# Kernel tuning notes

Measured on AMD Instinct MI355X. Metric: run time of the kernel, lower is better.

Reference implementation:

```python
import jax, jax.numpy as jnp
import numpy as np

L = 3
EPSILON = 0.01
T = 1.0
L1_EPS = 1e-12  # torch F.normalize default eps


def _cdist(x, y):
    # Euclidean pairwise distance, (b, n, d) x (b, m, d) -> (b, n, m)
    x2 = jnp.sum(x * x, axis=-1, keepdims=True)            # (b, n, 1)
    y2 = jnp.sum(y * y, axis=-1)[:, None, :]               # (b, 1, m)
    xy = jnp.einsum('bnd,bmd->bnm', x, y)                  # (b, n, m)
    return jnp.sqrt(jnp.maximum(x2 + y2 - 2.0 * xy, 0.0))


def setup_inputs() -> dict:
    key = jax.random.key(0)
    k1, k2 = jax.random.split(key)
    B, S, D = 4, 2048, 512
    A = jax.random.uniform(k1, (B, S, S), dtype=jnp.float32)
    V = jax.random.normal(k2, (B, S, D), dtype=jnp.float32)
    return {"A": A, "V": V}


def reference(A, V):
    M = jnp.matmul(A, V)  # (b, s, d)
    for _ in range(L):
        Md = jax.lax.stop_gradient(M)
        Vd = jax.lax.stop_gradient(V)
        dist = _cdist(Md, Vd)                               # (b, s, s)
        w = 1.0 / (dist + EPSILON)                          # norm == 'L2'
        ww = w * A                                          # (b, s, s)
        l1 = jnp.maximum(jnp.sum(jnp.abs(ww), axis=-1, keepdims=True), L1_EPS)
        ww_norm = ww / l1
        M = (1.0 - T) * M + T * jnp.matmul(ww_norm, V)
    return M
```

## Files before the change

### kernel.cpp

```cpp
#include <hip/hip_runtime.h>


typedef __bf16 bf16;
typedef bf16 bf16x4 __attribute__((ext_vector_type(4)));
typedef bf16 bf16x8 __attribute__((ext_vector_type(8)));
typedef float f32x4 __attribute__((ext_vector_type(4)));

#define S_DIM 2048
#define D_DIM 512
#define NB    4
#define EPSILON 0.01f

__global__ void cast_kernel(const float* __restrict__ in, bf16* __restrict__ out, int n4) {
  int i = blockIdx.x * blockDim.x + threadIdx.x;
  if (i >= n4) return;
  float4 v = ((const float4*)in)[i];
  bf16x4 o = { (bf16)v.x, (bf16)v.y, (bf16)v.z, (bf16)v.w };
  ((bf16x4*)out)[i] = o;
}

__global__ void transpose_cast_kernel(const float* __restrict__ V, bf16* __restrict__ Vt) {
  __shared__ float tile[64][68];
  int b  = blockIdx.z;
  int c0 = blockIdx.x * 64;
  int r0 = blockIdx.y * 64;
  const float* Vb = V  + (size_t)b * S_DIM * D_DIM;
  bf16*       Vtb = Vt + (size_t)b * S_DIM * D_DIM;
  int tx = threadIdx.x & 15, ty = threadIdx.x >> 4;
#pragma unroll
  for (int i = 0; i < 4; ++i) {
    int r = ty + i * 16;
    float4 v = *(const float4*)(Vb + (size_t)(r0 + r) * D_DIM + (c0 + tx * 4));
    tile[r][tx * 4 + 0] = v.x; tile[r][tx * 4 + 1] = v.y;
    tile[r][tx * 4 + 2] = v.z; tile[r][tx * 4 + 3] = v.w;
  }
  __syncthreads();
#pragma unroll
  for (int i = 0; i < 4; ++i) {
    int c = ty + i * 16;
    bf16x4 o = { (bf16)tile[tx * 4 + 0][c], (bf16)tile[tx * 4 + 1][c],
                 (bf16)tile[tx * 4 + 2][c], (bf16)tile[tx * 4 + 3][c] };
    *(bf16x4*)(Vtb + (size_t)(c0 + c) * S_DIM + (r0 + tx * 4)) = o;
  }
}

__global__ void rownorm_kernel(const bf16* __restrict__ X, float* __restrict__ out) {
  int row  = blockIdx.x * 4 + (threadIdx.x >> 6);
  int lane = threadIdx.x & 63;
  bf16x8 v = *(const bf16x8*)(X + (size_t)row * D_DIM + lane * 8);
  float s = 0.f;
#pragma unroll
  for (int i = 0; i < 8; ++i) { float f = (float)v[i]; s += f * f; }
#pragma unroll
  for (int off = 32; off > 0; off >>= 1) s += __shfl_down(s, off);
  if (lane == 0) out[row] = s;
}

template <int MODE>
__global__ __launch_bounds__(256, 4)
void gemm_kernel(const bf16* __restrict__ Amat, const bf16* __restrict__ Bmat,
                 int M, int N, int K,
                 bf16* __restrict__ Cp,
                 const float* __restrict__ m2, const float* __restrict__ v2,
                 const bf16* __restrict__ Aw, bf16* __restrict__ Wout,
                 float* __restrict__ l1) {
  int bz, ks, kbeg, kend;
  if (MODE == 4) { bz = blockIdx.z >> 1; ks = blockIdx.z & 1; kbeg = ks * (K >> 1); kend = kbeg + (K >> 1); }
  else           { bz = blockIdx.z;      ks = 0;              kbeg = 0;             kend = K; }
  const int row0 = blockIdx.y * 128;
  const int col0 = blockIdx.x * 128;
  const bf16* Ab = Amat + (size_t)bz * M * K;
  const bf16* Bb = Bmat + (size_t)bz * N * K;

  __shared__ char smem[32768];
  bf16*  ldsA = (bf16*)smem;
  bf16*  ldsB = (bf16*)(smem + 16384);
  float* ldsW = (float*)smem;

  const int tid  = threadIdx.x;
  const int wave = tid >> 6;
  const int lane = tid & 63;
  const int wr   = wave >> 1;
  const int wc   = wave & 1;
  const int q    = lane >> 4;
  const int c16  = lane & 15;

  const int srow = lane >> 3;
  const int scol = ((lane & 7) ^ srow) * 8;

  f32x4 acc[4][4] = {};

  for (int k0 = kbeg; k0 < kend; k0 += 64) {
#pragma unroll
    for (int i = 0; i < 4; ++i) {
      int slot = wave * 4 + i;
      int r = slot * 8 + srow;
      __builtin_amdgcn_global_load_lds(
          (const __attribute__((address_space(1))) void*)(Ab + (size_t)(row0 + r) * K + (k0 + scol)),
          (__attribute__((address_space(3))) void*)(ldsA + slot * 512), 16, 0, 0);
      __builtin_amdgcn_global_load_lds(
          (const __attribute__((address_space(1))) void*)(Bb + (size_t)(col0 + r) * K + (k0 + scol)),
          (__attribute__((address_space(3))) void*)(ldsB + slot * 512), 16, 0, 0);
    }
    __syncthreads();

#pragma unroll
    for (int kk = 0; kk < 2; ++kk) {
      bf16x8 afr[4], bfr[4];
#pragma unroll
      for (int mt = 0; mt < 4; ++mt) {
        int R = wr * 64 + mt * 16 + c16;
        int p = ((kk << 2) + q) ^ (c16 & 7);
        afr[mt] = *(const bf16x8*)(ldsA + (size_t)R * 64 + p * 8);
      }
#pragma unroll
      for (int nt = 0; nt < 4; ++nt) {
        int R = wc * 64 + nt * 16 + c16;
        int p = ((kk << 2) + q) ^ (c16 & 7);
        bfr[nt] = *(const bf16x8*)(ldsB + (size_t)R * 64 + p * 8);
      }
#pragma unroll
      for (int mt = 0; mt < 4; ++mt)
#pragma unroll
        for (int nt = 0; nt < 4; ++nt)
          acc[mt][nt] = __builtin_amdgcn_mfma_f32_16x16x32_bf16(afr[mt], bfr[nt], acc[mt][nt], 0, 0, 0);
    }
    __syncthreads();
  }

  const int rowBase = row0 + wr * 64 + q * 4;
  const int colBase = col0 + wc * 64 + c16;

  if (MODE == 1) {
    const float* m2b = m2 + (size_t)bz * M;
    const float* v2b = v2 + (size_t)bz * N;
    float v2v[4];
#pragma unroll
    for (int nt = 0; nt < 4; ++nt) v2v[nt] = v2b[colBase + nt * 16];
#pragma unroll
    for (int mt = 0; mt < 4; ++mt)
#pragma unroll
      for (int r = 0; r < 4; ++r) {
        float m2v = m2b[rowBase + mt * 16 + r];
#pragma unroll
        for (int nt = 0; nt < 4; ++nt) {
          float d2 = fmaxf(m2v + v2v[nt] - 2.f * acc[mt][nt][r], 0.f);
          acc[mt][nt][r] = __builtin_amdgcn_rcpf(__builtin_amdgcn_sqrtf(d2) + EPSILON);
        }
      }
  }

  const int lr  = tid >> 3;
  const int sub = tid & 7;
#pragma unroll
  for (int k = 0; k < 4; ++k) {
    __syncthreads();
    if (wr == (k >> 1)) {
#pragma unroll
      for (int m = 0; m < 2; ++m) {
        int mt = 2 * (k & 1) + m;
#pragma unroll
        for (int nt = 0; nt < 4; ++nt)
#pragma unroll
          for (int r = 0; r < 4; ++r)
            ldsW[(m * 16 + q * 4 + r) * 132 + wc * 64 + nt * 16 + c16] = acc[mt][nt][r];
      }
    }
    __syncthreads();
    int gi = row0 + 32 * k + lr;
    const float* wp = ldsW + lr * 132 + sub * 16;
    float4 w0 = *(const float4*)(wp + 0);
    float4 w1 = *(const float4*)(wp + 4);
    float4 w2 = *(const float4*)(wp + 8);
    float4 w3 = *(const float4*)(wp + 12);
    float wv_[16] = { w0.x, w0.y, w0.z, w0.w, w1.x, w1.y, w1.z, w1.w,
                      w2.x, w2.y, w2.z, w2.w, w3.x, w3.y, w3.z, w3.w };
    if (MODE == 1) {
      const bf16* Awb = Aw + (size_t)bz * M * N;
      bf16*       Wob = Wout + (size_t)bz * M * N;
      float*      l1b = l1 + (size_t)bz * M;
      const bf16* ap = Awb + (size_t)gi * N + (col0 + sub * 16);
      bf16x8 a0 = *(const bf16x8*)(ap);
      bf16x8 a1 = *(const bf16x8*)(ap + 8);
      bf16x8 o0, o1;
      float rs = 0.f;
#pragma unroll
      for (int e = 0; e < 8; ++e) {
        float x0 = wv_[e] * (float)a0[e];
        float x1 = wv_[e + 8] * (float)a1[e];
        o0[e] = (bf16)x0; o1[e] = (bf16)x1;
        rs += fabsf(x0) + fabsf(x1);
      }
      bf16* op = Wob + (size_t)gi * N + (col0 + sub * 16);
      *(bf16x8*)(op)     = o0;
      *(bf16x8*)(op + 8) = o1;
      rs += __shfl_xor(rs, 1);
      rs += __shfl_xor(rs, 2);
      rs += __shfl_xor(rs, 4);
      if (sub == 0) atomicAdd(&l1b[gi], rs);
    } else {
      bf16* Cb = Cp + ((size_t)ks * NB + bz) * ((size_t)M * N);
      bf16x8 o0, o1;
#pragma unroll
      for (int e = 0; e < 8; ++e) { o0[e] = (bf16)wv_[e]; o1[e] = (bf16)wv_[e + 8]; }
      bf16* op = Cb + (size_t)gi * N + (col0 + sub * 16);
      *(bf16x8*)(op)     = o0;
      *(bf16x8*)(op + 8) = o1;
    }
  }
}

template <int RMODE>
__global__ void reduce_kernel(const bf16* __restrict__ part, const float* __restrict__ l1,
                              bf16* __restrict__ Mo, float* __restrict__ Fo,
                              float* __restrict__ m2) {
  int wave = threadIdx.x >> 6, lane = threadIdx.x & 63;
  int rg = blockIdx.x * 4 + wave;
  const bf16* p0 = part + (size_t)rg * D_DIM + lane * 8;
  const bf16* p1 = p0 + (size_t)NB * S_DIM * D_DIM;
  bf16x8 a = *(const bf16x8*)p0;
  bf16x8 b = *(const bf16x8*)p1;
  float v[8];
#pragma unroll
  for (int e = 0; e < 8; ++e) v[e] = (float)a[e] + (float)b[e];
  float sc = 1.f;
  if (RMODE >= 1) sc = __builtin_amdgcn_rcpf(fmaxf(l1[rg], 1e-12f));
  float s = 0.f;
#pragma unroll
  for (int e = 0; e < 8; ++e) { v[e] *= sc; s += v[e] * v[e]; }
  if (RMODE == 2) {
    float4 o0 = { v[0], v[1], v[2], v[3] }, o1 = { v[4], v[5], v[6], v[7] };
    float* op = Fo + (size_t)rg * D_DIM + lane * 8;
    *(float4*)(op) = o0; *(float4*)(op + 4) = o1;
  } else {
    bf16x8 o;
#pragma unroll
    for (int e = 0; e < 8; ++e) o[e] = (bf16)v[e];
    *(bf16x8*)(Mo + (size_t)rg * D_DIM + lane * 8) = o;
#pragma unroll
    for (int off = 32; off > 0; off >>= 1) s += __shfl_xor(s, off);
    if (lane == 0) m2[rg] = s;
  }
}

extern "C" void kernel_launch(void* const* d_in, const int* in_sizes, int n_in,
                              void* d_out, int out_size, void* d_ws, size_t ws_size,
                              hipStream_t stream) {
  const float* A = (const float*)d_in[0];
  const float* V = (const float*)d_in[1];
  float* out = (float*)d_out;

  char* ws = (char*)d_ws;
  bf16* Abf = (bf16*)ws;   ws += (size_t)NB * S_DIM * S_DIM * 2;
  bf16* Vbf = (bf16*)ws;   ws += (size_t)NB * S_DIM * D_DIM * 2;
  bf16* Vt  = (bf16*)ws;   ws += (size_t)NB * S_DIM * D_DIM * 2;
  bf16* Mbf = (bf16*)ws;   ws += (size_t)NB * S_DIM * D_DIM * 2;
  bf16* Wbf = (bf16*)ws;   ws += (size_t)NB * S_DIM * S_DIM * 2;
  bf16* part = (bf16*)ws;  ws += (size_t)2 * NB * S_DIM * D_DIM * 2;
  float* v2 = (float*)ws;  ws += (size_t)NB * S_DIM * 4;
  float* m2 = (float*)ws;  ws += (size_t)NB * S_DIM * 4;
  float* l1 = (float*)ws;  ws += (size_t)NB * S_DIM * 4;

  int nA4 = NB * S_DIM * S_DIM / 4;
  int nV4 = NB * S_DIM * D_DIM / 4;
  cast_kernel<<<nA4 / 256, 256, 0, stream>>>(A, Abf, nA4);
  cast_kernel<<<nV4 / 256, 256, 0, stream>>>(V, Vbf, nV4);
  transpose_cast_kernel<<<dim3(D_DIM / 64, S_DIM / 64, NB), 256, 0, stream>>>(V, Vt);
  rownorm_kernel<<<NB * S_DIM / 4, 256, 0, stream>>>(Vbf, v2);

  gemm_kernel<4><<<dim3(D_DIM / 128, S_DIM / 128, NB * 2), 256, 0, stream>>>(
      Abf, Vt, S_DIM, D_DIM, S_DIM, part, nullptr, nullptr, nullptr, nullptr, nullptr);
  reduce_kernel<0><<<NB * S_DIM / 4, 256, 0, stream>>>(part, nullptr, Mbf, nullptr, m2);

  for (int it = 0; it < 3; ++it) {
    hipMemsetAsync(l1, 0, (size_t)NB * S_DIM * 4, stream);
    gemm_kernel<1><<<dim3(S_DIM / 128, S_DIM / 128, NB), 256, 0, stream>>>(
        Mbf, Vbf, S_DIM, S_DIM, D_DIM, nullptr, m2, v2, Abf, Wbf, l1);
    gemm_kernel<4><<<dim3(D_DIM / 128, S_DIM / 128, NB * 2), 256, 0, stream>>>(
        Wbf, Vt, S_DIM, D_DIM, S_DIM, part, nullptr, nullptr, nullptr, nullptr, nullptr);
    if (it < 2)
      reduce_kernel<1><<<NB * S_DIM / 4, 256, 0, stream>>>(part, l1, Mbf, nullptr, m2);
    else
      reduce_kernel<2><<<NB * S_DIM / 4, 256, 0, stream>>>(part, l1, nullptr, out, nullptr);
  }
}
```

Before: 354.5 us.

## Split-K four ways, prefetch A tiles early, replace l1 atomics with partials

The second GEMM's split-K factor goes from 2 to 4, giving 512 blocks instead of 256 so the GPU's CUs are better filled, and the reduce kernel now sums four bf16 partials. The fused distance GEMM loads its A-weight tiles before and during the main loop so their latency overlaps compute, instead of loading them in the epilogue. The l1 row sums are written as per-column-block partials and summed in the reduce kernel, which removes the memset and the atomics. The cost is extra partial-buffer traffic, extra register pressure from the prefetched tiles, and more reads in the reduce step.

```diff
diff --git a/kernel.cpp b/kernel.cpp
--- a/kernel.cpp
+++ b/kernel.cpp
@@ -63,9 +63,9 @@
                  bf16* __restrict__ Cp,
                  const float* __restrict__ m2, const float* __restrict__ v2,
                  const bf16* __restrict__ Aw, bf16* __restrict__ Wout,
-                 float* __restrict__ l1) {
+                 float* __restrict__ l1p) {
   int bz, ks, kbeg, kend;
-  if (MODE == 4) { bz = blockIdx.z >> 1; ks = blockIdx.z & 1; kbeg = ks * (K >> 1); kend = kbeg + (K >> 1); }
+  if (MODE == 4) { bz = blockIdx.z >> 2; ks = blockIdx.z & 3; kbeg = ks * (K >> 2); kend = kbeg + (K >> 2); }
   else           { bz = blockIdx.z;      ks = 0;              kbeg = 0;             kend = K; }
   const int row0 = blockIdx.y * 128;
   const int col0 = blockIdx.x * 128;
@@ -87,6 +87,20 @@
 
   const int srow = lane >> 3;
   const int scol = ((lane & 7) ^ srow) * 8;
+
+  const int lr  = tid >> 3;
+  const int sub = tid & 7;
+
+  const bf16* Awb = (MODE == 1) ? (Aw + (size_t)bz * M * N) : nullptr;
+  bf16x8 apA[2], apB[2];
+  if (MODE == 1) {
+#pragma unroll
+    for (int k = 0; k < 2; ++k) {
+      const bf16* ap = Awb + (size_t)(row0 + 32 * k + lr) * N + (col0 + sub * 16);
+      apA[k] = *(const bf16x8*)(ap);
+      apB[k] = *(const bf16x8*)(ap + 8);
+    }
+  }
 
   f32x4 acc[4][4] = {};
 
@@ -131,7 +145,14 @@
   const int rowBase = row0 + wr * 64 + q * 4;
   const int colBase = col0 + wc * 64 + c16;
 
+  bf16x8 apA2[2], apB2[2];
   if (MODE == 1) {
+#pragma unroll
+    for (int k = 0; k < 2; ++k) {
+      const bf16* ap = Awb + (size_t)(row0 + 32 * (k + 2) + lr) * N + (col0 + sub * 16);
+      apA2[k] = *(const bf16x8*)(ap);
+      apB2[k] = *(const bf16x8*)(ap + 8);
+    }
     const float* m2b = m2 + (size_t)bz * M;
     const float* v2b = v2 + (size_t)bz * N;
     float v2v[4];
@@ -150,8 +171,6 @@
       }
   }
 
-  const int lr  = tid >> 3;
-  const int sub = tid & 7;
 #pragma unroll
   for (int k = 0; k < 4; ++k) {
     __syncthreads();
@@ -176,12 +195,8 @@
     float wv_[16] = { w0.x, w0.y, w0.z, w0.w, w1.x, w1.y, w1.z, w1.w,
                       w2.x, w2.y, w2.z, w2.w, w3.x, w3.y, w3.z, w3.w };
     if (MODE == 1) {
-      const bf16* Awb = Aw + (size_t)bz * M * N;
-      bf16*       Wob = Wout + (size_t)bz * M * N;
-      float*      l1b = l1 + (size_t)bz * M;
-      const bf16* ap = Awb + (size_t)gi * N + (col0 + sub * 16);
-      bf16x8 a0 = *(const bf16x8*)(ap);
-      bf16x8 a1 = *(const bf16x8*)(ap + 8);
+      bf16x8 a0 = (k < 2) ? apA[k] : apA2[k - 2];
+      bf16x8 a1 = (k < 2) ? apB[k] : apB2[k - 2];
       bf16x8 o0, o1;
       float rs = 0.f;
 #pragma unroll
@@ -191,13 +206,13 @@
         o0[e] = (bf16)x0; o1[e] = (bf16)x1;
         rs += fabsf(x0) + fabsf(x1);
       }
-      bf16* op = Wob + (size_t)gi * N + (col0 + sub * 16);
+      bf16* op = Wout + (size_t)bz * M * N + (size_t)gi * N + (col0 + sub * 16);
       *(bf16x8*)(op)     = o0;
       *(bf16x8*)(op + 8) = o1;
       rs += __shfl_xor(rs, 1);
       rs += __shfl_xor(rs, 2);
       rs += __shfl_xor(rs, 4);
-      if (sub == 0) atomicAdd(&l1b[gi], rs);
+      if (sub == 0) l1p[((size_t)blockIdx.x * NB + bz) * M + gi] = rs;
     } else {
       bf16* Cb = Cp + ((size_t)ks * NB + bz) * ((size_t)M * N);
       bf16x8 o0, o1;
@@ -211,20 +226,26 @@
 }
 
 template <int RMODE>
-__global__ void reduce_kernel(const bf16* __restrict__ part, const float* __restrict__ l1,
+__global__ void reduce_kernel(const bf16* __restrict__ part, const float* __restrict__ l1p,
                               bf16* __restrict__ Mo, float* __restrict__ Fo,
                               float* __restrict__ m2) {
   int wave = threadIdx.x >> 6, lane = threadIdx.x & 63;
   int rg = blockIdx.x * 4 + wave;
-  const bf16* p0 = part + (size_t)rg * D_DIM + lane * 8;
-  const bf16* p1 = p0 + (size_t)NB * S_DIM * D_DIM;
-  bf16x8 a = *(const bf16x8*)p0;
-  bf16x8 b = *(const bf16x8*)p1;
-  float v[8];
-#pragma unroll
-  for (int e = 0; e < 8; ++e) v[e] = (float)a[e] + (float)b[e];
+  float v[8] = {};
+#pragma unroll
+  for (int ks = 0; ks < 4; ++ks) {
+    bf16x8 a = *(const bf16x8*)(part + (size_t)ks * NB * S_DIM * D_DIM + (size_t)rg * D_DIM + lane * 8);
+#pragma unroll
+    for (int e = 0; e < 8; ++e) v[e] += (float)a[e];
+  }
   float sc = 1.f;
-  if (RMODE >= 1) sc = __builtin_amdgcn_rcpf(fmaxf(l1[rg], 1e-12f));
+  if (RMODE >= 1) {
+    int b = rg >> 11, row = rg & (S_DIM - 1);
+    float l1v = 0.f;
+#pragma unroll
+    for (int e = 0; e < 16; ++e) l1v += l1p[((size_t)e * NB + b) * S_DIM + row];
+    sc = __builtin_amdgcn_rcpf(fmaxf(l1v, 1e-12f));
+  }
   float s = 0.f;
 #pragma unroll
   for (int e = 0; e < 8; ++e) { v[e] *= sc; s += v[e] * v[e]; }
@@ -256,10 +277,10 @@
   bf16* Vt  = (bf16*)ws;   ws += (size_t)NB * S_DIM * D_DIM * 2;
   bf16* Mbf = (bf16*)ws;   ws += (size_t)NB * S_DIM * D_DIM * 2;
   bf16* Wbf = (bf16*)ws;   ws += (size_t)NB * S_DIM * S_DIM * 2;
-  bf16* part = (bf16*)ws;  ws += (size_t)2 * NB * S_DIM * D_DIM * 2;
+  bf16* part = (bf16*)ws;  ws += (size_t)4 * NB * S_DIM * D_DIM * 2;
   float* v2 = (float*)ws;  ws += (size_t)NB * S_DIM * 4;
   float* m2 = (float*)ws;  ws += (size_t)NB * S_DIM * 4;
-  float* l1 = (float*)ws;  ws += (size_t)NB * S_DIM * 4;
+  float* l1p = (float*)ws; ws += (size_t)16 * NB * S_DIM * 4;
 
   int nA4 = NB * S_DIM * S_DIM / 4;
   int nV4 = NB * S_DIM * D_DIM / 4;
@@ -268,19 +289,18 @@
   transpose_cast_kernel<<<dim3(D_DIM / 64, S_DIM / 64, NB), 256, 0, stream>>>(V, Vt);
   rownorm_kernel<<<NB * S_DIM / 4, 256, 0, stream>>>(Vbf, v2);
 
-  gemm_kernel<4><<<dim3(D_DIM / 128, S_DIM / 128, NB * 2), 256, 0, stream>>>(
+  gemm_kernel<4><<<dim3(D_DIM / 128, S_DIM / 128, NB * 4), 256, 0, stream>>>(
       Abf, Vt, S_DIM, D_DIM, S_DIM, part, nullptr, nullptr, nullptr, nullptr, nullptr);
   reduce_kernel<0><<<NB * S_DIM / 4, 256, 0, stream>>>(part, nullptr, Mbf, nullptr, m2);
 
   for (int it = 0; it < 3; ++it) {
-    hipMemsetAsync(l1, 0, (size_t)NB * S_DIM * 4, stream);
     gemm_kernel<1><<<dim3(S_DIM / 128, S_DIM / 128, NB), 256, 0, stream>>>(
-        Mbf, Vbf, S_DIM, S_DIM, D_DIM, nullptr, m2, v2, Abf, Wbf, l1);
-    gemm_kernel<4><<<dim3(D_DIM / 128, S_DIM / 128, NB * 2), 256, 0, stream>>>(
+        Mbf, Vbf, S_DIM, S_DIM, D_DIM, nullptr, m2, v2, Abf, Wbf, l1p);
+    gemm_kernel<4><<<dim3(D_DIM / 128, S_DIM / 128, NB * 4), 256, 0, stream>>>(
         Wbf, Vt, S_DIM, D_DIM, S_DIM, part, nullptr, nullptr, nullptr, nullptr, nullptr);
     if (it < 2)
-      reduce_kernel<1><<<NB * S_DIM / 4, 256, 0, stream>>>(part, l1, Mbf, nullptr, m2);
+      reduce_kernel<1><<<NB * S_DIM / 4, 256, 0, stream>>>(part, l1p, Mbf, nullptr, m2);
     else
-      reduce_kernel<2><<<NB * S_DIM / 4, 256, 0, stream>>>(part, l1, nullptr, out, nullptr);
-  }
-}
+      reduce_kernel<2><<<NB * S_DIM / 4, 256, 0, stream>>>(part, l1p, nullptr, out, nullptr);
+  }
+}
```

Measured after the change: 371.4 us. 4.8% more time.
